# Kernel optimization log

Measured on AMD Instinct MI355X. Metric: run time of the kernel, lower is better.

The kernel has to match this reference:

```python
import jax, jax.numpy as jnp
import numpy as np

N = 10000
E = 160000
DIMS = [256, 256, 256, 256]
EPS = 1e-5
DSCALE = 1.0
SPE_IDX = 0


def setup_inputs() -> dict:
    key = jax.random.key(0)
    ks = jax.random.split(key, 40)
    inp = {}
    inp['x'] = jax.random.normal(ks[0], (N, DIMS[0]), dtype=jnp.float32)
    inp['src'] = jax.random.randint(ks[1], (E,), 0, N, dtype=jnp.int32)
    inp['dst'] = jax.random.randint(ks[2], (E,), 0, N, dtype=jnp.int32)
    k = 3
    for i, (din, dout) in enumerate(zip(DIMS[:-1], DIMS[1:])):
        s = 1.0 / np.sqrt(din)
        inp[f'Ws{i}'] = jax.random.uniform(ks[k], (din, dout), jnp.float32, -s, s); k += 1
        inp[f'Wn{i}'] = jax.random.uniform(ks[k], (din, dout), jnp.float32, -s, s); k += 1
        inp[f'b{i}'] = jnp.zeros((dout,), jnp.float32)
        inp[f'g{i}'] = jnp.ones((dout,), jnp.float32)
        inp[f'be{i}'] = jnp.zeros((dout,), jnp.float32)
    return inp


def _sage(h, src, dst, Ws, Wn, b):
    # mean aggregation over in-neighbors: segment-sum gathered src feats over dst
    agg = jax.ops.segment_sum(h[src], dst, num_segments=N)          # [N, din]
    deg = jax.ops.segment_sum(jnp.ones((E,), h.dtype), dst, num_segments=N)
    mean = agg / jnp.maximum(deg, 1.0)[:, None]
    return h @ Ws + mean @ Wn + b


def _bn(h, g, be):
    # BatchNorm1d, training mode (biased batch variance)
    mu = jnp.mean(h, axis=0)
    var = jnp.mean((h - mu) ** 2, axis=0)
    return (h - mu) * jax.lax.rsqrt(var + EPS) * g + be


def reference(x, src, dst, Ws0, Wn0, b0, g0, be0, Ws1, Wn1, b1, g1, be1,
              Ws2, Wn2, b2, g2, be2):
    params = [(Ws0, Wn0, b0, g0, be0), (Ws1, Wn1, b1, g1, be1),
              (Ws2, Wn2, b2, g2, be2)]
    n_layers = len(params)
    outs = x
    for i, (Ws, Wn, b, g, be) in enumerate(params):
        outs = _sage(outs, src, dst, Ws, Wn, b)
        # hid side-outputs (sigmoid(outs*dscale)[spe_idx]) don't affect outs path
        outs = _bn(outs, g, be)
        if i != n_layers - 1:
            outs = jax.nn.relu(outs)
        else:
            outs = jax.nn.sigmoid(outs)
    return outs
```

## Files before the change

### kernel.cpp

```cpp
#include <hip/hip_runtime.h>
#include <math.h>

#define NN 10000
#define EE 160000
#define DIM 256
#define KK 512
#define CAP 128
#define EPS_BN 1e-5f
#define AST 516

typedef __attribute__((ext_vector_type(8)))  short bf16x8;
typedef __attribute__((ext_vector_type(16))) float f32x16;

union U16 { uint2 u2[2]; bf16x8 v; };

static __device__ __forceinline__ unsigned short f2bf(float f) {
    unsigned u = __float_as_uint(f);
    unsigned r = (u + 0x7fffu + ((u >> 16) & 1u)) >> 16;
    return (unsigned short)r;
}
static __device__ __forceinline__ float bflo(unsigned v) { return __uint_as_float(v << 16); }
static __device__ __forceinline__ float bfhi(unsigned v) { return __uint_as_float(v & 0xffff0000u); }
static __device__ __forceinline__ unsigned packbf(float a, float b) {
    return (unsigned)f2bf(a) | ((unsigned)f2bf(b) << 16);
}

struct Params {
    const float* x; const int* src; const int* dst;
    const float *Ws0, *Wn0, *Ws1, *Wn1, *Ws2, *Wn2;
    const float *g0, *be0, *g1, *be1, *g2, *be2;
    float* out;
    unsigned short* hx;
    unsigned short* z0;
    unsigned short* z1;
    unsigned short* wcat;
    float* stats;
    int* cnt;
    int* slots;
};

static __device__ __forceinline__ void accum8(float* a, uint4 v) {
    a[0] += bflo(v.x); a[1] += bfhi(v.x);
    a[2] += bflo(v.y); a[3] += bfhi(v.y);
    a[4] += bflo(v.z); a[5] += bfhi(v.z);
    a[6] += bflo(v.w); a[7] += bfhi(v.w);
}
static __device__ __forceinline__ void accum8n(float* a, uint4 v,
                                               const float* sc, const float* sh) {
    a[0] += fmaxf(bflo(v.x) * sc[0] + sh[0], 0.f);
    a[1] += fmaxf(bfhi(v.x) * sc[1] + sh[1], 0.f);
    a[2] += fmaxf(bflo(v.y) * sc[2] + sh[2], 0.f);
    a[3] += fmaxf(bfhi(v.y) * sc[3] + sh[3], 0.f);
    a[4] += fmaxf(bflo(v.z) * sc[4] + sh[4], 0.f);
    a[5] += fmaxf(bfhi(v.z) * sc[5] + sh[5], 0.f);
    a[6] += fmaxf(bflo(v.w) * sc[6] + sh[6], 0.f);
    a[7] += fmaxf(bfhi(v.w) * sc[7] + sh[7], 0.f);
}

__global__ __launch_bounds__(256) void k_prep(Params P) {
    int g0 = blockIdx.x * 256 + threadIdx.x;
    int stride = gridDim.x * 256;
    for (int g = g0; g < NN * 64; g += stride) {
        int r = g >> 6, c4 = (g & 63) * 4;
        float4 v = *(const float4*)(P.x + (size_t)r * DIM + c4);
        uint2 p; p.x = packbf(v.x, v.y); p.y = packbf(v.z, v.w);
        *(uint2*)(P.hx + (size_t)r * DIM + c4) = p;
    }
    for (int g = g0; g < 3 * DIM * KK; g += stride) {
        int L = g >> 17; int i = g & 131071;
        int k = i >> 8, n = i & 255;
        const float* Ws = (L == 0) ? P.Ws0 : ((L == 1) ? P.Ws1 : P.Ws2);
        const float* Wn = (L == 0) ? P.Wn0 : ((L == 1) ? P.Wn1 : P.Wn2);
        float v = (k < DIM) ? Ws[(size_t)k * DIM + n] : Wn[(size_t)(k - DIM) * DIM + n];
        P.wcat[(size_t)L * DIM * KK + (size_t)n * KK + k] = f2bf(v);
    }
    for (int g = g0; g < NN + 6 * DIM; g += stride) {
        if (g < NN) P.cnt[g] = 0;
        else P.stats[g - NN] = 0.f;
    }
}

__global__ __launch_bounds__(256) void k_bucket(Params P) {
    int e = blockIdx.x * 256 + threadIdx.x;
    if (e < EE) {
        int d = P.dst[e];
        int p = atomicAdd(&P.cnt[d], 1);
        if (p < CAP) P.slots[(size_t)d * CAP + p] = P.src[e];
    }
}

__global__ __launch_bounds__(512) void k_ag(Params P, int L,
                                            const unsigned short* __restrict__ gsrc,
                                            unsigned short* __restrict__ gdst) {
    __shared__ unsigned short At[32][AST];
    int t = threadIdx.x;
    int wave = t >> 6, lane = t & 63;
    int h = lane >> 5, l = lane & 31;

    float sc[8], sh[8];
    if (L > 0) {
        const float* st = P.stats + (L - 1) * 2 * DIM;
        const float* gam = (L == 1) ? P.g0 : P.g1;
        const float* bet = (L == 1) ? P.be0 : P.be1;
#pragma unroll
        for (int i = 0; i < 8; ++i) {
            int c = l * 8 + i;
            float mu  = st[c] * (1.0f / NN);
            float var = st[DIM + c] * (1.0f / NN) - mu * mu;
            float k = rsqrtf(var + EPS_BN) * gam[c];
            sc[i] = k;
            sh[i] = bet[c] - mu * k;
        }
    }
    const uint4* srcm = (const uint4*)gsrc;

    for (int i = 0; i < 4; ++i) {
        int m = wave * 4 + i;
        int node = blockIdx.x * 32 + m;
        unsigned short* arow = &At[m][0];
        if (node >= NN) {
            if (h == 0) {
                uint2 z2 = make_uint2(0u, 0u);
                *(uint2*)(arow + l * 8)           = z2;
                *(uint2*)(arow + l * 8 + 4)       = z2;
                *(uint2*)(arow + 256 + l * 8)     = z2;
                *(uint2*)(arow + 256 + l * 8 + 4) = z2;
            }
            continue;
        }
        int cnt = P.cnt[node]; if (cnt > CAP) cnt = CAP;
        const int* sl = P.slots + (size_t)node * CAP;
        if (h == 0) {
            uint4 z = srcm[(size_t)node * 32 + l];
            uint4 o;
            if (L > 0) {
                o.x = packbf(fmaxf(bflo(z.x) * sc[0] + sh[0], 0.f),
                             fmaxf(bfhi(z.x) * sc[1] + sh[1], 0.f));
                o.y = packbf(fmaxf(bflo(z.y) * sc[2] + sh[2], 0.f),
                             fmaxf(bfhi(z.y) * sc[3] + sh[3], 0.f));
                o.z = packbf(fmaxf(bflo(z.z) * sc[4] + sh[4], 0.f),
                             fmaxf(bfhi(z.z) * sc[5] + sh[5], 0.f));
                o.w = packbf(fmaxf(bflo(z.w) * sc[6] + sh[6], 0.f),
                             fmaxf(bfhi(z.w) * sc[7] + sh[7], 0.f));
            } else o = z;
            *(uint2*)(arow + l * 8)     = make_uint2(o.x, o.y);
            *(uint2*)(arow + l * 8 + 4) = make_uint2(o.z, o.w);
        }
        float a[8] = {0, 0, 0, 0, 0, 0, 0, 0};
        int j = h;
        if (L == 0) {
            for (; j + 6 < cnt; j += 8) {
                int i0 = sl[j],     i1 = sl[j + 2];
                int i2 = sl[j + 4], i3 = sl[j + 6];
                uint4 v0 = srcm[(size_t)i0 * 32 + l];
                uint4 v1 = srcm[(size_t)i1 * 32 + l];
                uint4 v2 = srcm[(size_t)i2 * 32 + l];
                uint4 v3 = srcm[(size_t)i3 * 32 + l];
                accum8(a, v0); accum8(a, v1); accum8(a, v2); accum8(a, v3);
            }
            for (; j < cnt; j += 2) accum8(a, srcm[(size_t)sl[j] * 32 + l]);
        } else {
            for (; j + 6 < cnt; j += 8) {
                int i0 = sl[j],     i1 = sl[j + 2];
                int i2 = sl[j + 4], i3 = sl[j + 6];
                uint4 v0 = srcm[(size_t)i0 * 32 + l];
                uint4 v1 = srcm[(size_t)i1 * 32 + l];
                uint4 v2 = srcm[(size_t)i2 * 32 + l];
                uint4 v3 = srcm[(size_t)i3 * 32 + l];
                accum8n(a, v0, sc, sh); accum8n(a, v1, sc, sh);
                accum8n(a, v2, sc, sh); accum8n(a, v3, sc, sh);
            }
            for (; j < cnt; j += 2) accum8n(a, srcm[(size_t)sl[j] * 32 + l], sc, sh);
        }
#pragma unroll
        for (int q = 0; q < 8; ++q) a[q] += __shfl_xor(a[q], 32);
        if (h == 0) {
            float inv = 1.0f / (float)(cnt > 1 ? cnt : 1);
            *(uint2*)(arow + 256 + l * 8)     = make_uint2(packbf(a[0] * inv, a[1] * inv),
                                                           packbf(a[2] * inv, a[3] * inv));
            *(uint2*)(arow + 256 + l * 8 + 4) = make_uint2(packbf(a[4] * inv, a[5] * inv),
                                                           packbf(a[6] * inv, a[7] * inv));
        }
    }
    __syncthreads();

    const unsigned short* wcatL = P.wcat + (size_t)L * DIM * KK;
    float* statsL = P.stats + L * 2 * DIM;
    int m = l;
    int row0 = blockIdx.x * 32;
    int colw0 = wave * 32;
    const unsigned short* Bp = wcatL + (size_t)(colw0 + m) * KK + h * 8;
    const unsigned short* Arow = &At[m][0];
    f32x16 acc;
#pragma unroll
    for (int i = 0; i < 16; ++i) acc[i] = 0.f;
#pragma unroll 8
    for (int k0 = 0; k0 < KK; k0 += 16) {
        U16 ua;
        ua.u2[0] = *(const uint2*)(Arow + k0 + h * 8);
        ua.u2[1] = *(const uint2*)(Arow + k0 + h * 8 + 4);
        bf16x8 av = ua.v;
        bf16x8 bv = *(const bf16x8*)(Bp + k0);
        acc = __builtin_amdgcn_mfma_f32_32x32x16_bf16(av, bv, acc, 0, 0, 0);
    }
    int cc = colw0 + m;
    float s = 0.f, s2 = 0.f;
#pragma unroll
    for (int reg = 0; reg < 16; ++reg) {
        int r = row0 + (reg & 3) + 8 * (reg >> 2) + 4 * h;
        if (r < NN) {
            float v = acc[reg];
            gdst[(size_t)r * DIM + cc] = f2bf(v);
            s += v; s2 += v * v;
        }
    }
    s  += __shfl_down(s, 32);
    s2 += __shfl_down(s2, 32);
    if (h == 0) {
        atomicAdd(&statsL[cc], s);
        atomicAdd(&statsL[DIM + cc], s2);
    }
}

__global__ __launch_bounds__(256) void k_norm(Params P) {
    const float* statsL = P.stats + 2 * 2 * DIM;
    int t = threadIdx.x;
    int c8 = (t & 31) * 8;
    int r = blockIdx.x * 8 + (t >> 5);
    float sc[8], sh[8];
#pragma unroll
    for (int i = 0; i < 8; ++i) {
        int c = c8 + i;
        float mu  = statsL[c] * (1.0f / NN);
        float var = statsL[DIM + c] * (1.0f / NN) - mu * mu;
        float k = rsqrtf(var + EPS_BN) * P.g2[c];
        sc[i] = k;
        sh[i] = P.be2[c] - mu * k;
    }
    uint4 v = *(const uint4*)(P.z0 + (size_t)r * DIM + c8);
    float f[8] = {bflo(v.x), bfhi(v.x), bflo(v.y), bfhi(v.y),
                  bflo(v.z), bfhi(v.z), bflo(v.w), bfhi(v.w)};
#pragma unroll
    for (int i = 0; i < 8; ++i) f[i] = f[i] * sc[i] + sh[i];
    float4 o0, o1;
    o0.x = 1.0f / (1.0f + __expf(-f[0]));
    o0.y = 1.0f / (1.0f + __expf(-f[1]));
    o0.z = 1.0f / (1.0f + __expf(-f[2]));
    o0.w = 1.0f / (1.0f + __expf(-f[3]));
    o1.x = 1.0f / (1.0f + __expf(-f[4]));
    o1.y = 1.0f / (1.0f + __expf(-f[5]));
    o1.z = 1.0f / (1.0f + __expf(-f[6]));
    o1.w = 1.0f / (1.0f + __expf(-f[7]));
    *(float4*)(P.out + (size_t)r * DIM + c8)     = o0;
    *(float4*)(P.out + (size_t)r * DIM + c8 + 4) = o1;
}

extern "C" void kernel_launch(void* const* d_in, const int* in_sizes, int n_in,
                              void* d_out, int out_size, void* d_ws, size_t ws_size,
                              hipStream_t stream) {
    Params P;
    P.x   = (const float*)d_in[0];
    P.src = (const int*)d_in[1];
    P.dst = (const int*)d_in[2];
    P.Ws0 = (const float*)d_in[3];  P.Wn0 = (const float*)d_in[4];
    P.g0  = (const float*)d_in[6];  P.be0 = (const float*)d_in[7];
    P.Ws1 = (const float*)d_in[8];  P.Wn1 = (const float*)d_in[9];
    P.g1  = (const float*)d_in[11]; P.be1 = (const float*)d_in[12];
    P.Ws2 = (const float*)d_in[13]; P.Wn2 = (const float*)d_in[14];
    P.g2  = (const float*)d_in[16]; P.be2 = (const float*)d_in[17];
    P.out = (float*)d_out;

    char* ws = (char*)d_ws;
    size_t off = 0;
    P.hx   = (unsigned short*)(ws + off); off += (size_t)NN * DIM * 2;
    P.z0   = (unsigned short*)(ws + off); off += (size_t)NN * DIM * 2;
    P.z1   = (unsigned short*)(ws + off); off += (size_t)NN * DIM * 2;
    P.wcat = (unsigned short*)(ws + off); off += (size_t)3 * DIM * KK * 2;
    P.stats = (float*)(ws + off); off += 3 * 2 * DIM * sizeof(float);
    P.cnt   = (int*)(ws + off); off += (size_t)NN * 4; off = (off + 255) & ~(size_t)255;
    P.slots = (int*)(ws + off); off += (size_t)NN * CAP * 4;
    (void)ws_size;

    k_prep<<<512, 256, 0, stream>>>(P);
    k_bucket<<<(EE + 255) / 256, 256, 0, stream>>>(P);
    k_ag<<<313, 512, 0, stream>>>(P, 0, P.hx, P.z0);
    k_ag<<<313, 512, 0, stream>>>(P, 1, P.z0, P.z1);
    k_ag<<<313, 512, 0, stream>>>(P, 2, P.z1, P.z0);
    k_norm<<<NN / 8, 256, 0, stream>>>(P);
}
```

Baseline: 224.2 us.

## Halve rows per block and switch GEMM to 16x16x32 MFMA tiles

Each k_ag block now handles 16 nodes instead of 32, which doubles the grid to 626 blocks and spreads the gather-heavy aggregation across more CUs. The fused GEMM stage changes from one 32x32x16 MFMA per wave to two 16x16x32 MFMAs covering 32 columns. The BN stats reduction is rewritten to match the new accumulator layout. In exchange, each block reloads the full weight slice for half as many rows, doubling weight traffic and the number of stat atomics.

Result: slower. 255.9 us (+14.1%).

```diff
diff --git a/kernel.cpp b/kernel.cpp
--- a/kernel.cpp
+++ b/kernel.cpp
@@ -9,8 +9,8 @@
 #define EPS_BN 1e-5f
 #define AST 516
 
-typedef __attribute__((ext_vector_type(8)))  short bf16x8;
-typedef __attribute__((ext_vector_type(16))) float f32x16;
+typedef __attribute__((ext_vector_type(8))) short bf16x8;
+typedef __attribute__((ext_vector_type(4))) float f32x4;
 
 union U16 { uint2 u2[2]; bf16x8 v; };
 
@@ -92,7 +92,7 @@
 __global__ __launch_bounds__(512) void k_ag(Params P, int L,
                                             const unsigned short* __restrict__ gsrc,
                                             unsigned short* __restrict__ gdst) {
-    __shared__ unsigned short At[32][AST];
+    __shared__ unsigned short At[16][AST];
     int t = threadIdx.x;
     int wave = t >> 6, lane = t & 63;
     int h = lane >> 5, l = lane & 31;
@@ -114,9 +114,9 @@
     }
     const uint4* srcm = (const uint4*)gsrc;
 
-    for (int i = 0; i < 4; ++i) {
-        int m = wave * 4 + i;
-        int node = blockIdx.x * 32 + m;
+    for (int i = 0; i < 2; ++i) {
+        int m = wave * 2 + i;
+        int node = blockIdx.x * 16 + m;
         unsigned short* arow = &At[m][0];
         if (node >= NN) {
             if (h == 0) {
@@ -150,23 +150,19 @@
         int j = h;
         if (L == 0) {
             for (; j + 6 < cnt; j += 8) {
-                int i0 = sl[j],     i1 = sl[j + 2];
-                int i2 = sl[j + 4], i3 = sl[j + 6];
-                uint4 v0 = srcm[(size_t)i0 * 32 + l];
-                uint4 v1 = srcm[(size_t)i1 * 32 + l];
-                uint4 v2 = srcm[(size_t)i2 * 32 + l];
-                uint4 v3 = srcm[(size_t)i3 * 32 + l];
+                uint4 v0 = srcm[(size_t)sl[j + 0] * 32 + l];
+                uint4 v1 = srcm[(size_t)sl[j + 2] * 32 + l];
+                uint4 v2 = srcm[(size_t)sl[j + 4] * 32 + l];
+                uint4 v3 = srcm[(size_t)sl[j + 6] * 32 + l];
                 accum8(a, v0); accum8(a, v1); accum8(a, v2); accum8(a, v3);
             }
             for (; j < cnt; j += 2) accum8(a, srcm[(size_t)sl[j] * 32 + l]);
         } else {
             for (; j + 6 < cnt; j += 8) {
-                int i0 = sl[j],     i1 = sl[j + 2];
-                int i2 = sl[j + 4], i3 = sl[j + 6];
-                uint4 v0 = srcm[(size_t)i0 * 32 + l];
-                uint4 v1 = srcm[(size_t)i1 * 32 + l];
-                uint4 v2 = srcm[(size_t)i2 * 32 + l];
-                uint4 v3 = srcm[(size_t)i3 * 32 + l];
+                uint4 v0 = srcm[(size_t)sl[j + 0] * 32 + l];
+                uint4 v1 = srcm[(size_t)sl[j + 2] * 32 + l];
+                uint4 v2 = srcm[(size_t)sl[j + 4] * 32 + l];
+                uint4 v3 = srcm[(size_t)sl[j + 6] * 32 + l];
                 accum8n(a, v0, sc, sh); accum8n(a, v1, sc, sh);
                 accum8n(a, v2, sc, sh); accum8n(a, v3, sc, sh);
             }
@@ -186,39 +182,46 @@
 
     const unsigned short* wcatL = P.wcat + (size_t)L * DIM * KK;
     float* statsL = P.stats + L * 2 * DIM;
-    int m = l;
-    int row0 = blockIdx.x * 32;
+    int n16 = lane & 15;
+    int q   = lane >> 4;
+    int row0 = blockIdx.x * 16;
     int colw0 = wave * 32;
-    const unsigned short* Bp = wcatL + (size_t)(colw0 + m) * KK + h * 8;
-    const unsigned short* Arow = &At[m][0];
-    f32x16 acc;
-#pragma unroll
-    for (int i = 0; i < 16; ++i) acc[i] = 0.f;
+    const unsigned short* Arow = &At[n16][0];
+    const unsigned short* Bp0 = wcatL + (size_t)(colw0 + n16) * KK + q * 8;
+    const unsigned short* Bp1 = Bp0 + (size_t)16 * KK;
+    f32x4 acc0, acc1;
+#pragma unroll
+    for (int i = 0; i < 4; ++i) { acc0[i] = 0.f; acc1[i] = 0.f; }
 #pragma unroll 8
-    for (int k0 = 0; k0 < KK; k0 += 16) {
+    for (int k0 = 0; k0 < KK; k0 += 32) {
         U16 ua;
-        ua.u2[0] = *(const uint2*)(Arow + k0 + h * 8);
-        ua.u2[1] = *(const uint2*)(Arow + k0 + h * 8 + 4);
+        ua.u2[0] = *(const uint2*)(Arow + k0 + q * 8);
+        ua.u2[1] = *(const uint2*)(Arow + k0 + q * 8 + 4);
         bf16x8 av = ua.v;
-        bf16x8 bv = *(const bf16x8*)(Bp + k0);
-        acc = __builtin_amdgcn_mfma_f32_32x32x16_bf16(av, bv, acc, 0, 0, 0);
-    }
-    int cc = colw0 + m;
-    float s = 0.f, s2 = 0.f;
-#pragma unroll
-    for (int reg = 0; reg < 16; ++reg) {
-        int r = row0 + (reg & 3) + 8 * (reg >> 2) + 4 * h;
-        if (r < NN) {
-            float v = acc[reg];
-            gdst[(size_t)r * DIM + cc] = f2bf(v);
-            s += v; s2 += v * v;
-        }
-    }
-    s  += __shfl_down(s, 32);
-    s2 += __shfl_down(s2, 32);
-    if (h == 0) {
-        atomicAdd(&statsL[cc], s);
-        atomicAdd(&statsL[DIM + cc], s2);
+        bf16x8 b0 = *(const bf16x8*)(Bp0 + k0);
+        bf16x8 b1 = *(const bf16x8*)(Bp1 + k0);
+        acc0 = __builtin_amdgcn_mfma_f32_16x16x32_bf16(av, b0, acc0, 0, 0, 0);
+        acc1 = __builtin_amdgcn_mfma_f32_16x16x32_bf16(av, b1, acc1, 0, 0, 0);
+    }
+#pragma unroll
+    for (int ct = 0; ct < 2; ++ct) {
+        int cc = colw0 + ct * 16 + n16;
+        float s = 0.f, s2 = 0.f;
+#pragma unroll
+        for (int reg = 0; reg < 4; ++reg) {
+            int r = row0 + q * 4 + reg;
+            if (r < NN) {
+                float v = (ct == 0) ? acc0[reg] : acc1[reg];
+                gdst[(size_t)r * DIM + cc] = f2bf(v);
+                s += v; s2 += v * v;
+            }
+        }
+        s  += __shfl_xor(s, 16);  s  += __shfl_xor(s, 32);
+        s2 += __shfl_xor(s2, 16); s2 += __shfl_xor(s2, 32);
+        if (lane < 16) {
+            atomicAdd(&statsL[cc], s);
+            atomicAdd(&statsL[DIM + cc], s2);
+        }
     }
 }
 
@@ -283,8 +286,8 @@
 
     k_prep<<<512, 256, 0, stream>>>(P);
     k_bucket<<<(EE + 255) / 256, 256, 0, stream>>>(P);
-    k_ag<<<313, 512, 0, stream>>>(P, 0, P.hx, P.z0);
-    k_ag<<<313, 512, 0, stream>>>(P, 1, P.z0, P.z1);
-    k_ag<<<313, 512, 0, stream>>>(P, 2, P.z1, P.z0);
+    k_ag<<<626, 512, 0, stream>>>(P, 0, P.hx, P.z0);
+    k_ag<<<626, 512, 0, stream>>>(P, 1, P.z0, P.z1);
+    k_ag<<<626, 512, 0, stream>>>(P, 2, P.z1, P.z0);
     k_norm<<<NN / 8, 256, 0, stream>>>(P);
 }
```
